# Performance work log

Measured on AMD Instinct MI355X. Metric: run time of the kernel, lower is better.

## Reference

```python
import jax, jax.numpy as jnp
import numpy as np

DIM_MODEL = 1024
NUM_HEADS = 16
HEAD_DIM = DIM_MODEL // NUM_HEADS
NEG_INF = -1e9


def setup_inputs() -> dict:
    key = jax.random.key(0)
    ks = jax.random.split(key, 12)
    B, S = 4, 2048
    s = 1.0 / np.sqrt(DIM_MODEL)
    inp = {
        "query": jax.random.normal(ks[0], (B, S, DIM_MODEL), jnp.float32),
        "key": jax.random.normal(ks[1], (B, S, DIM_MODEL), jnp.float32),
        "value": jax.random.normal(ks[2], (B, S, DIM_MODEL), jnp.float32),
        "mask": jax.random.randint(ks[3], (B, 1, S, S), 0, 2, jnp.int32),
        "Wq": jax.random.normal(ks[4], (DIM_MODEL, DIM_MODEL), jnp.float32) * s,
        "bq": jnp.zeros((DIM_MODEL,), jnp.float32),
        "Wk": jax.random.normal(ks[5], (DIM_MODEL, DIM_MODEL), jnp.float32) * s,
        "bk": jnp.zeros((DIM_MODEL,), jnp.float32),
        "Wv": jax.random.normal(ks[6], (DIM_MODEL, DIM_MODEL), jnp.float32) * s,
        "bv": jnp.zeros((DIM_MODEL,), jnp.float32),
        "Wo": jax.random.normal(ks[7], (DIM_MODEL, DIM_MODEL), jnp.float32) * s,
        "bo": jnp.zeros((DIM_MODEL,), jnp.float32),
    }
    return inp


def _split_heads(x, B):
    # [B, S, D] -> [B, H, S, Dh]
    S = x.shape[1]
    return x.reshape(B, S, NUM_HEADS, HEAD_DIM).transpose(0, 2, 1, 3)


def reference(query, key, value, mask, Wq, bq, Wk, bk, Wv, bv, Wo, bo):
    B = query.shape[0]
    q = _split_heads(query @ Wq + bq, B)   # [B,H,Sq,Dh]
    k = _split_heads(key @ Wk + bk, B)     # [B,H,Sk,Dh]
    v = _split_heads(value @ Wv + bv, B)   # [B,H,Sk,Dh]

    scale = 1.0 / np.sqrt(HEAD_DIM)
    scores = jnp.einsum("bhqd,bhkd->bhqk", q, k) * scale  # [B,H,Sq,Sk]
    scores = jnp.where(mask == 0, NEG_INF, scores)
    probs = jax.nn.softmax(scores, axis=-1)
    attn = jnp.einsum("bhqk,bhkd->bhqd", probs, v)         # [B,H,Sq,Dh]

    attn = attn.transpose(0, 2, 1, 3).reshape(B, -1, DIM_MODEL)  # [B,Sq,D]
    return attn @ Wo + bo
```

## Files before the change

### kernel.cpp

```cpp
#include <hip/hip_runtime.h>


typedef unsigned short u16;
typedef _Float16 f16;
typedef __attribute__((ext_vector_type(8))) _Float16 half8;
typedef __attribute__((ext_vector_type(8))) unsigned short u16x8;
typedef __attribute__((ext_vector_type(4))) unsigned short u16x4;
typedef __attribute__((ext_vector_type(4))) float floatx4;

__device__ f16 g_Bt[4][1024 * 1024];
__device__ f16 g_X[3][8192 * 1024];
__device__ f16 g_Qh[8192 * 1024];
__device__ f16 g_Kh[8192 * 1024];
__device__ f16 g_Vh[8192 * 1024];
__device__ f16 g_Oh[8192 * 1024];
__device__ u16 g_pbias[(size_t)4 * 2048 * 2048];
__device__ int g_is_bf16;

__device__ __forceinline__ float bf2f(u16 u) {
  union { unsigned int i; float f; } v;
  v.i = ((unsigned int)u) << 16;
  return v.f;
}
__device__ __forceinline__ u16 f2h_bits(float f) {
  union { _Float16 h; u16 u; } v;
  v.h = (_Float16)f;
  return v.u;
}

__global__ void detect_kernel(const u16* __restrict__ q) {
  if (threadIdx.x == 0) {
    int cnt = 0;
    for (int i = 0; i < 256; ++i) {
      const u16 v = q[i];
      const int e = (v >> 7) & 0xFF;
      cnt += ((e >= 100 && e <= 135) || ((v & 0x7FFF) == 0)) ? 1 : 0;
    }
    g_is_bf16 = (cnt >= 205) ? 1 : 0;
  }
}

__device__ __forceinline__ float load_in(const void* p, size_t i) {
  return g_is_bf16 ? bf2f(((const u16*)p)[i]) : ((const float*)p)[i];
}

__device__ __forceinline__ int swz128(int row, int cb) {
  return row * 128 + (cb ^ ((row & 7) << 4));
}
__device__ __forceinline__ int swz(int row, int cb) {
  return ((row << 6) + cb) ^ ((row & 7) << 4);
}

__device__ __forceinline__ void gl_lds16(void* g, void* l) {
  __builtin_amdgcn_global_load_lds(
      (__attribute__((address_space(1))) void*)g,
      (__attribute__((address_space(3))) void*)l, 16, 0, 0);
}

__global__ __launch_bounds__(256) void cvt_kernel(
    const void* __restrict__ q, const void* __restrict__ k,
    const void* __restrict__ v) {
  const int z = blockIdx.y;
  const void* x = (z == 0) ? q : (z == 1) ? k : v;
  f16* oh = g_X[z];
  const size_t i = ((size_t)blockIdx.x * 256 + threadIdx.x) * 8;
  half8 h;
  if (!g_is_bf16) {
    const float* xf = (const float*)x + i;
    const float4 a = *(const float4*)xf;
    const float4 b = *(const float4*)(xf + 4);
    h[0] = (f16)a.x; h[1] = (f16)a.y; h[2] = (f16)a.z; h[3] = (f16)a.w;
    h[4] = (f16)b.x; h[5] = (f16)b.y; h[6] = (f16)b.z; h[7] = (f16)b.w;
  } else {
    const u16x8 a = *(const u16x8*)((const u16*)x + i);
#pragma unroll
    for (int j = 0; j < 8; ++j) h[j] = (f16)bf2f(a[j]);
  }
  *(half8*)(oh + i) = h;
}

__global__ __launch_bounds__(256) void maskbias_kernel(const int* __restrict__ mask) {
  const size_t tid = (size_t)blockIdx.x * 256 + threadIdx.x;
  const size_t base = tid * 4;
  const int b = (int)(base >> 22);
  const size_t rem = base & 0x3FFFFFu;
  const int row = (int)(rem >> 11);
  const int c0 = (int)(rem & 2047);
  const int4 m = *(const int4*)(mask + base);
  const int tile = c0 >> 6;
  const int cl = c0 & 63;
  const int lan = cl & 15;
  const int ni = cl >> 4;
  u16* dst = g_pbias + ((size_t)b << 22) + ((size_t)row << 11) + tile * 64 + ni;
  const u16 NEG = 0xCE6E;
  dst[(lan + 0) * 4] = m.x ? (u16)0 : NEG;
  dst[(lan + 1) * 4] = m.y ? (u16)0 : NEG;
  dst[(lan + 2) * 4] = m.z ? (u16)0 : NEG;
  dst[(lan + 3) * 4] = m.w ? (u16)0 : NEG;
}

__global__ void wtrans_kernel(const void* __restrict__ in, int wo) {
  __shared__ float tile[32][33];
  const int tx = threadIdx.x, ty = threadIdx.y;
  const int n0 = blockIdx.x * 32, k0 = blockIdx.y * 32;
  tile[ty][tx] = load_in(in, (size_t)(k0 + ty) * 1024 + n0 + tx);
  __syncthreads();
  g_Bt[wo][(size_t)(n0 + ty) * 1024 + k0 + tx] = (f16)tile[tx][ty];
}

#define GEMM_CORE(AP, BP)                                                    \
  const int t = threadIdx.x;                                                 \
  const int lane = t & 63;                                                   \
  const int lanelo = lane & 15;                                              \
  const int quad = lane >> 4;                                                \
  const int wave = t >> 6;                                                   \
  const int wr = wave >> 1, wc = wave & 1;                                   \
  const int bm = blockIdx.x * 128;                                           \
  const int bn = blockIdx.y * 128;                                           \
         \
  const int s4 = lane << 4;                                                  \
  const int rl = s4 ^ ((s4 >> 2) & 0x70) ^ ((s4 >> 4) & 0x10);               \
  const int r0 = wave * 16 + (rl >> 6);            \
  const int cbb = rl & 63;                             \
  const char* pA0 = (const char*)(AP) + (size_t)(bm + r0) * 2048 + cbb;      \
  const char* pA1 = pA0 + (size_t)64 * 2048;                                 \
  const char* pB0 = (const char*)(BP) + (size_t)(bn + r0) * 2048 + cbb;      \
  const char* pB1 = pB0 + (size_t)64 * 2048;                                 \
  u16* lA0 = &As[wave * 512]; u16* lA1 = &As[2048 + wave * 512];             \
  u16* lB0 = &Bs[wave * 512]; u16* lB1 = &Bs[2048 + wave * 512];             \
  floatx4 acc[4][4];                                                         \
  _Pragma("unroll") for (int i = 0; i < 4; ++i)                              \
      _Pragma("unroll") for (int j = 0; j < 4; ++j) acc[i][j] = (floatx4)(0.f); \
  for (int k0 = 0; k0 < 1024; k0 += 32) {                                    \
    __syncthreads();                              \
    const size_t kb = (size_t)(k0 << 1);                                     \
    gl_lds16((void*)(pA0 + kb), lA0);                                        \
    gl_lds16((void*)(pA1 + kb), lA1);                                        \
    gl_lds16((void*)(pB0 + kb), lB0);                                        \
    gl_lds16((void*)(pB1 + kb), lB1);                                        \
    __syncthreads();       \
    half8 af[4], bf_[4];                                                     \
    _Pragma("unroll") for (int mi = 0; mi < 4; ++mi) {                       \
      const int row = wr * 64 + mi * 16 + lanelo;                            \
      af[mi] = *(const half8*)&As[swz(row, quad * 16) >> 1];                 \
    }                                                                        \
    _Pragma("unroll") for (int ni = 0; ni < 4; ++ni) {                       \
      const int row = wc * 64 + ni * 16 + lanelo;                            \
      bf_[ni] = *(const half8*)&Bs[swz(row, quad * 16) >> 1];                \
    }                                                                        \
    _Pragma("unroll") for (int mi = 0; mi < 4; ++mi)                         \
        _Pragma("unroll") for (int ni = 0; ni < 4; ++ni)                     \
      acc[mi][ni] = __builtin_amdgcn_mfma_f32_16x16x32_f16(                  \
          af[mi], bf_[ni], acc[mi][ni], 0, 0, 0);                            \
  }

__global__ __launch_bounds__(256) void gemm_qkv_kernel(
    const void* __restrict__ bq, const void* __restrict__ bk,
    const void* __restrict__ bv) {
  __shared__ __align__(16) u16 As[4096];
  __shared__ __align__(16) u16 Bs[4096];
  const int z = blockIdx.z;
  const void* bias = (z == 0) ? bq : (z == 1) ? bk : bv;
  f16* Ch = (z == 0) ? g_Qh : (z == 1) ? g_Kh : g_Vh;

  GEMM_CORE(g_X[z], g_Bt[z])

#pragma unroll
  for (int ni = 0; ni < 4; ++ni) {
    const int col = bn + wc * 64 + ni * 16 + lanelo;
    const float bvv = load_in(bias, col);
#pragma unroll
    for (int mi = 0; mi < 4; ++mi) {
#pragma unroll
      for (int rg = 0; rg < 4; ++rg) {
        const int row = bm + wr * 64 + mi * 16 + quad * 4 + rg;
        Ch[(size_t)row * 1024 + col] = (f16)(acc[mi][ni][rg] + bvv);
      }
    }
  }
}

__global__ __launch_bounds__(256) void gemm_o_kernel(
    const void* __restrict__ bias, float* __restrict__ Cptr) {
  __shared__ __align__(16) u16 As[4096];
  __shared__ __align__(16) u16 Bs[4096];

  GEMM_CORE(g_Oh, g_Bt[3])

#pragma unroll
  for (int ni = 0; ni < 4; ++ni) {
    const int col = bn + wc * 64 + ni * 16 + lanelo;
    const float bvv = load_in(bias, col);
#pragma unroll
    for (int mi = 0; mi < 4; ++mi) {
#pragma unroll
      for (int rg = 0; rg < 4; ++rg) {
        const int row = bm + wr * 64 + mi * 16 + quad * 4 + rg;
        Cptr[(size_t)row * 1024 + col] = acc[mi][ni][rg] + bvv;
      }
    }
  }
}

__global__ __launch_bounds__(512, 4) void attn_mfma_kernel() {
  constexpr int S = 2048, D = 1024, NT = S / 64;
  __shared__ __align__(16) u16 k_s[64 * 64];
  __shared__ __align__(16) u16 vt_s[64 * 64];
  __shared__ __align__(16) u16 p_s[128 * 64];

  const int t = threadIdx.x;
  const int lane = t & 63;
  const int lanelo = lane & 15;
  const int quad = lane >> 4;
  const int wave = t >> 6;

  const int q0 = blockIdx.x * 128;
  const int h = blockIdx.y;
  const int b = blockIdx.z;
  const size_t bh = (size_t)b * S * D + (size_t)h * 64;

  half8 a_q[2];
#pragma unroll
  for (int kk = 0; kk < 2; ++kk)
    a_q[kk] = *(const half8*)(g_Qh + bh +
        (size_t)(q0 + wave * 16 + lanelo) * D + kk * 32 + quad * 8);

  half8 b_ones;
#pragma unroll
  for (int j = 0; j < 8; ++j)
    b_ones[j] = (lanelo == 0) ? (f16)1.0f : (f16)0.0f;

  const int sj = t & 63;
  const int scc = (t >> 6) * 8;

  const u16* Kbase = (const u16*)g_Kh + bh + (size_t)sj * D + scc;
  const u16* Vbase = (const u16*)g_Vh + bh + (size_t)sj * D + scc;
  u16x8 kreg = *(const u16x8*)(Kbase);
  u16x8 vreg = *(const u16x8*)(Vbase);

  floatx4 o_acc[4];
#pragma unroll
  for (int ni = 0; ni < 4; ++ni) o_acc[ni] = (floatx4)(0.f);
  floatx4 o_l = (floatx4)(0.f);

  const u16* pbrow = g_pbias + ((size_t)b << 22) +
                     ((size_t)(q0 + wave * 16 + quad * 4) << 11) + (lanelo << 2);

  for (int kt = 0; kt < NT; ++kt) {
    const int j0 = kt * 64;
    __syncthreads();

    *(u16x8*)&k_s[swz128(sj, scc * 2) >> 1] = kreg;
#pragma unroll
    for (int u = 0; u < 8; ++u)
      vt_s[swz128(scc + u, sj * 2) >> 1] = vreg[u];
    __syncthreads();

    {
      const int ktn = (kt + 1 < NT) ? kt + 1 : kt;
      kreg = *(const u16x8*)(Kbase + (size_t)ktn * 64 * D);
      vreg = *(const u16x8*)(Vbase + (size_t)ktn * 64 * D);
    }
    u16x4 bs[4];
#pragma unroll
    for (int r = 0; r < 4; ++r)
      bs[r] = *(const u16x4*)(pbrow + ((size_t)r << 11) + j0);

    floatx4 sacc[4];
#pragma unroll
    for (int ni = 0; ni < 4; ++ni) sacc[ni] = (floatx4)(0.f);
#pragma unroll
    for (int kk = 0; kk < 2; ++kk) {
#pragma unroll
      for (int ni = 0; ni < 4; ++ni) {
        const half8 bb = *(const half8*)
            &k_s[swz128(ni * 16 + lanelo, kk * 64 + quad * 16) >> 1];
        sacc[ni] = __builtin_amdgcn_mfma_f32_16x16x32_f16(a_q[kk], bb, sacc[ni], 0, 0, 0);
      }
    }

#pragma unroll
    for (int r = 0; r < 4; ++r) {
      const int prow = wave * 16 + quad * 4 + r;
#pragma unroll
      for (int ni = 0; ni < 4; ++ni) {
        const float s = sacc[ni][r] * 0.125f + bf2f(bs[r][ni]);
        p_s[swz128(prow, (ni * 16 + lanelo) * 2) >> 1] = f2h_bits(__expf(s));
      }
    }
    asm volatile("s_waitcnt lgkmcnt(0)" ::: "memory");
    __builtin_amdgcn_sched_barrier(0);

#pragma unroll
    for (int kk = 0; kk < 2; ++kk) {
      const half8 a_p = *(const half8*)
          &p_s[swz128(wave * 16 + lanelo, kk * 64 + quad * 16) >> 1];
#pragma unroll
      for (int ni = 0; ni < 4; ++ni) {
        const half8 bb = *(const half8*)
            &vt_s[swz128(ni * 16 + lanelo, kk * 64 + quad * 16) >> 1];
        o_acc[ni] = __builtin_amdgcn_mfma_f32_16x16x32_f16(a_p, bb, o_acc[ni], 0, 0, 0);
      }
      o_l = __builtin_amdgcn_mfma_f32_16x16x32_f16(a_p, b_ones, o_l, 0, 0, 0);
    }
  }

#pragma unroll
  for (int r = 0; r < 4; ++r) {
    const float lsum = __shfl(o_l[r], lane & 48);
    const float inv = 1.f / lsum;
    const int row = q0 + wave * 16 + quad * 4 + r;
#pragma unroll
    for (int ni = 0; ni < 4; ++ni)
      g_Oh[bh + (size_t)row * D + ni * 16 + lanelo] = (f16)(o_acc[ni][r] * inv);
  }
}

extern "C" void kernel_launch(void* const* d_in, const int* in_sizes, int n_in,
                              void* d_out, int out_size, void* d_ws, size_t ws_size,
                              hipStream_t stream) {
  const void* query = d_in[0];
  const void* key   = d_in[1];
  const void* value = d_in[2];
  const int* mask   = (const int*)d_in[3];
  const void* Wq = d_in[4];
  const void* bq = d_in[5];
  const void* Wk = d_in[6];
  const void* bk = d_in[7];
  const void* Wv = d_in[8];
  const void* bv = d_in[9];
  const void* Wo = d_in[10];
  const void* bo = d_in[11];

  detect_kernel<<<1, 64, 0, stream>>>((const u16*)query);

  maskbias_kernel<<<16384, 256, 0, stream>>>(mask);

  dim3 tb(32, 32), tg(32, 32);
  wtrans_kernel<<<tg, tb, 0, stream>>>(Wq, 0);
  wtrans_kernel<<<tg, tb, 0, stream>>>(Wk, 1);
  wtrans_kernel<<<tg, tb, 0, stream>>>(Wv, 2);
  wtrans_kernel<<<tg, tb, 0, stream>>>(Wo, 3);

  cvt_kernel<<<dim3(4096, 3), 256, 0, stream>>>(query, key, value);

  gemm_qkv_kernel<<<dim3(64, 8, 3), 256, 0, stream>>>(bq, bk, bv);

  attn_mfma_kernel<<<dim3(16, 16, 4), 512, 0, stream>>>();

  gemm_o_kernel<<<dim3(64, 8), 256, 0, stream>>>(bo, (float*)d_out);
}
```

Measured before the change: 514.7 us.

## Double-buffer K/V tiles in attention and merge weight transposes into one launch

```diff
diff --git a/kernel.cpp b/kernel.cpp
--- a/kernel.cpp
+++ b/kernel.cpp
@@ -99,8 +99,13 @@
   dst[(lan + 3) * 4] = m.w ? (u16)0 : NEG;
 }
 
-__global__ void wtrans_kernel(const void* __restrict__ in, int wo) {
+__global__ void wtrans_kernel(const void* __restrict__ Wq,
+                              const void* __restrict__ Wk,
+                              const void* __restrict__ Wv,
+                              const void* __restrict__ Wo) {
   __shared__ float tile[32][33];
+  const int wo = blockIdx.z;
+  const void* in = (wo == 0) ? Wq : (wo == 1) ? Wk : (wo == 2) ? Wv : Wo;
   const int tx = threadIdx.x, ty = threadIdx.y;
   const int n0 = blockIdx.x * 32, k0 = blockIdx.y * 32;
   tile[ty][tx] = load_in(in, (size_t)(k0 + ty) * 1024 + n0 + tx);
@@ -204,8 +209,8 @@
 
 __global__ __launch_bounds__(512, 4) void attn_mfma_kernel() {
   constexpr int S = 2048, D = 1024, NT = S / 64;
-  __shared__ __align__(16) u16 k_s[64 * 64];
-  __shared__ __align__(16) u16 vt_s[64 * 64];
+  __shared__ __align__(16) u16 k_s[2][64 * 64];
+  __shared__ __align__(16) u16 vt_s[2][64 * 64];
   __shared__ __align__(16) u16 p_s[128 * 64];
 
   const int t = threadIdx.x;
@@ -232,35 +237,33 @@
 
   const int sj = t & 63;
   const int scc = (t >> 6) * 8;
+  const int koff = swz128(sj, scc * 2) >> 1;
 
   const u16* Kbase = (const u16*)g_Kh + bh + (size_t)sj * D + scc;
   const u16* Vbase = (const u16*)g_Vh + bh + (size_t)sj * D + scc;
+
+  floatx4 o_acc[4];
+#pragma unroll
+  for (int ni = 0; ni < 4; ++ni) o_acc[ni] = (floatx4)(0.f);
+  floatx4 o_l = (floatx4)(0.f);
+
+  const u16* pbrow = g_pbias + ((size_t)b << 22) +
+                     ((size_t)(q0 + wave * 16 + quad * 4) << 11) + (lanelo << 2);
+
   u16x8 kreg = *(const u16x8*)(Kbase);
   u16x8 vreg = *(const u16x8*)(Vbase);
-
-  floatx4 o_acc[4];
-#pragma unroll
-  for (int ni = 0; ni < 4; ++ni) o_acc[ni] = (floatx4)(0.f);
-  floatx4 o_l = (floatx4)(0.f);
-
-  const u16* pbrow = g_pbias + ((size_t)b << 22) +
-                     ((size_t)(q0 + wave * 16 + quad * 4) << 11) + (lanelo << 2);
+  *(u16x8*)&k_s[0][koff] = kreg;
+#pragma unroll
+  for (int u = 0; u < 8; ++u)
+    vt_s[0][swz128(scc + u, sj * 2) >> 1] = vreg[u];
+  kreg = *(const u16x8*)(Kbase + (size_t)64 * D);
+  vreg = *(const u16x8*)(Vbase + (size_t)64 * D);
+  __syncthreads();
 
   for (int kt = 0; kt < NT; ++kt) {
+    const int cur = kt & 1;
     const int j0 = kt * 64;
-    __syncthreads();
-
-    *(u16x8*)&k_s[swz128(sj, scc * 2) >> 1] = kreg;
-#pragma unroll
-    for (int u = 0; u < 8; ++u)
-      vt_s[swz128(scc + u, sj * 2) >> 1] = vreg[u];
-    __syncthreads();
-
-    {
-      const int ktn = (kt + 1 < NT) ? kt + 1 : kt;
-      kreg = *(const u16x8*)(Kbase + (size_t)ktn * 64 * D);
-      vreg = *(const u16x8*)(Vbase + (size_t)ktn * 64 * D);
-    }
+
     u16x4 bs[4];
 #pragma unroll
     for (int r = 0; r < 4; ++r)
@@ -274,9 +277,20 @@
 #pragma unroll
       for (int ni = 0; ni < 4; ++ni) {
         const half8 bb = *(const half8*)
-            &k_s[swz128(ni * 16 + lanelo, kk * 64 + quad * 16) >> 1];
+            &k_s[cur][swz128(ni * 16 + lanelo, kk * 64 + quad * 16) >> 1];
         sacc[ni] = __builtin_amdgcn_mfma_f32_16x16x32_f16(a_q[kk], bb, sacc[ni], 0, 0, 0);
       }
+    }
+
+    if (kt + 1 < NT) {
+      const int nxt = cur ^ 1;
+      *(u16x8*)&k_s[nxt][koff] = kreg;
+#pragma unroll
+      for (int u = 0; u < 8; ++u)
+        vt_s[nxt][swz128(scc + u, sj * 2) >> 1] = vreg[u];
+      const size_t koff2 = (size_t)((kt + 2 < NT) ? kt + 2 : NT - 1) * 64 * D;
+      kreg = *(const u16x8*)(Kbase + koff2);
+      vreg = *(const u16x8*)(Vbase + koff2);
     }
 
 #pragma unroll
@@ -298,11 +312,13 @@
 #pragma unroll
       for (int ni = 0; ni < 4; ++ni) {
         const half8 bb = *(const half8*)
-            &vt_s[swz128(ni * 16 + lanelo, kk * 64 + quad * 16) >> 1];
+            &vt_s[cur][swz128(ni * 16 + lanelo, kk * 64 + quad * 16) >> 1];
         o_acc[ni] = __builtin_amdgcn_mfma_f32_16x16x32_f16(a_p, bb, o_acc[ni], 0, 0, 0);
       }
       o_l = __builtin_amdgcn_mfma_f32_16x16x32_f16(a_p, b_ones, o_l, 0, 0, 0);
     }
+
+    __syncthreads();
   }
 
 #pragma unroll
@@ -336,11 +352,7 @@
 
   maskbias_kernel<<<16384, 256, 0, stream>>>(mask);
 
-  dim3 tb(32, 32), tg(32, 32);
-  wtrans_kernel<<<tg, tb, 0, stream>>>(Wq, 0);
-  wtrans_kernel<<<tg, tb, 0, stream>>>(Wk, 1);
-  wtrans_kernel<<<tg, tb, 0, stream>>>(Wv, 2);
-  wtrans_kernel<<<tg, tb, 0, stream>>>(Wo, 3);
+  wtrans_kernel<<<dim3(32, 32, 4), dim3(32, 32), 0, stream>>>(Wq, Wk, Wv, Wo);
 
   cvt_kernel<<<dim3(4096, 3), 256, 0, stream>>>(query, key, value);
 
```

Measured after the change: 517.4 us. No clear change (+0.5%).

## Pre-transpose V per head and fold softmax scale into Q projection

Applied to the files above, without the earlier changes.

```diff
diff --git a/kernel.cpp b/kernel.cpp
--- a/kernel.cpp
+++ b/kernel.cpp
@@ -13,6 +13,7 @@
 __device__ f16 g_Qh[8192 * 1024];
 __device__ f16 g_Kh[8192 * 1024];
 __device__ f16 g_Vh[8192 * 1024];
+__device__ f16 g_Vt[(size_t)4 * 16 * 64 * 2048];
 __device__ f16 g_Oh[8192 * 1024];
 __device__ u16 g_pbias[(size_t)4 * 2048 * 2048];
 __device__ int g_is_bf16;
@@ -99,13 +100,37 @@
   dst[(lan + 3) * 4] = m.w ? (u16)0 : NEG;
 }
 
-__global__ void wtrans_kernel(const void* __restrict__ in, int wo) {
+__global__ void wtrans_kernel(const void* __restrict__ Wq,
+                              const void* __restrict__ Wk,
+                              const void* __restrict__ Wv,
+                              const void* __restrict__ Wo) {
   __shared__ float tile[32][33];
+  const int wo = blockIdx.z;
+  const void* in = (wo == 0) ? Wq : (wo == 1) ? Wk : (wo == 2) ? Wv : Wo;
   const int tx = threadIdx.x, ty = threadIdx.y;
   const int n0 = blockIdx.x * 32, k0 = blockIdx.y * 32;
   tile[ty][tx] = load_in(in, (size_t)(k0 + ty) * 1024 + n0 + tx);
   __syncthreads();
   g_Bt[wo][(size_t)(n0 + ty) * 1024 + k0 + tx] = (f16)tile[tx][ty];
+}
+
+__global__ __launch_bounds__(512) void vtrans_kernel() {
+  __shared__ f16 tile[64][65];
+  const int tx = threadIdx.x, ty = threadIdx.y;
+  const int t0 = blockIdx.x * 64;
+  const int h = blockIdx.y;
+  const int b = blockIdx.z;
+#pragma unroll
+  for (int i = 0; i < 8; ++i) {
+    const int row = ty + i * 8;
+    tile[row][tx] = g_Vh[(size_t)(b * 2048 + t0 + row) * 1024 + h * 64 + tx];
+  }
+  __syncthreads();
+#pragma unroll
+  for (int i = 0; i < 8; ++i) {
+    const int d = ty + i * 8;
+    g_Vt[((size_t)(b * 16 + h) * 64 + d) * 2048 + t0 + tx] = tile[tx][d];
+  }
 }
 
 #define GEMM_CORE(AP, BP)                                                    \
@@ -165,6 +190,7 @@
 
   GEMM_CORE(g_X[z], g_Bt[z])
 
+  const float sc_ = (z == 0) ? 0.125f : 1.0f;
 #pragma unroll
   for (int ni = 0; ni < 4; ++ni) {
     const int col = bn + wc * 64 + ni * 16 + lanelo;
@@ -174,7 +200,7 @@
 #pragma unroll
       for (int rg = 0; rg < 4; ++rg) {
         const int row = bm + wr * 64 + mi * 16 + quad * 4 + rg;
-        Ch[(size_t)row * 1024 + col] = (f16)(acc[mi][ni][rg] + bvv);
+        Ch[(size_t)row * 1024 + col] = (f16)((acc[mi][ni][rg] + bvv) * sc_);
       }
     }
   }
@@ -232,9 +258,11 @@
 
   const int sj = t & 63;
   const int scc = (t >> 6) * 8;
+  const int koff = swz128(sj, scc * 2) >> 1;
 
   const u16* Kbase = (const u16*)g_Kh + bh + (size_t)sj * D + scc;
-  const u16* Vbase = (const u16*)g_Vh + bh + (size_t)sj * D + scc;
+  const u16* Vbase = (const u16*)g_Vt +
+                     ((size_t)(b * 16 + h) * 64 + sj) * 2048 + scc;
   u16x8 kreg = *(const u16x8*)(Kbase);
   u16x8 vreg = *(const u16x8*)(Vbase);
 
@@ -250,16 +278,14 @@
     const int j0 = kt * 64;
     __syncthreads();
 
-    *(u16x8*)&k_s[swz128(sj, scc * 2) >> 1] = kreg;
-#pragma unroll
-    for (int u = 0; u < 8; ++u)
-      vt_s[swz128(scc + u, sj * 2) >> 1] = vreg[u];
+    *(u16x8*)&k_s[koff] = kreg;
+    *(u16x8*)&vt_s[koff] = vreg;
     __syncthreads();
 
     {
       const int ktn = (kt + 1 < NT) ? kt + 1 : kt;
       kreg = *(const u16x8*)(Kbase + (size_t)ktn * 64 * D);
-      vreg = *(const u16x8*)(Vbase + (size_t)ktn * 64 * D);
+      vreg = *(const u16x8*)(Vbase + (size_t)ktn * 64);
     }
     u16x4 bs[4];
 #pragma unroll
@@ -268,7 +294,10 @@
 
     floatx4 sacc[4];
 #pragma unroll
-    for (int ni = 0; ni < 4; ++ni) sacc[ni] = (floatx4)(0.f);
+    for (int ni = 0; ni < 4; ++ni) {
+#pragma unroll
+      for (int r = 0; r < 4; ++r) sacc[ni][r] = bf2f(bs[r][ni]);
+    }
 #pragma unroll
     for (int kk = 0; kk < 2; ++kk) {
 #pragma unroll
@@ -284,8 +313,8 @@
       const int prow = wave * 16 + quad * 4 + r;
 #pragma unroll
       for (int ni = 0; ni < 4; ++ni) {
-        const float s = sacc[ni][r] * 0.125f + bf2f(bs[r][ni]);
-        p_s[swz128(prow, (ni * 16 + lanelo) * 2) >> 1] = f2h_bits(__expf(s));
+        p_s[swz128(prow, (ni * 16 + lanelo) * 2) >> 1] =
+            f2h_bits(__expf(sacc[ni][r]));
       }
     }
     asm volatile("s_waitcnt lgkmcnt(0)" ::: "memory");
@@ -336,16 +365,14 @@
 
   maskbias_kernel<<<16384, 256, 0, stream>>>(mask);
 
-  dim3 tb(32, 32), tg(32, 32);
-  wtrans_kernel<<<tg, tb, 0, stream>>>(Wq, 0);
-  wtrans_kernel<<<tg, tb, 0, stream>>>(Wk, 1);
-  wtrans_kernel<<<tg, tb, 0, stream>>>(Wv, 2);
-  wtrans_kernel<<<tg, tb, 0, stream>>>(Wo, 3);
+  wtrans_kernel<<<dim3(32, 32, 4), dim3(32, 32), 0, stream>>>(Wq, Wk, Wv, Wo);
 
   cvt_kernel<<<dim3(4096, 3), 256, 0, stream>>>(query, key, value);
 
   gemm_qkv_kernel<<<dim3(64, 8, 3), 256, 0, stream>>>(bq, bk, bv);
 
+  vtrans_kernel<<<dim3(32, 16, 4), dim3(64, 8), 0, stream>>>();
+
   attn_mfma_kernel<<<dim3(16, 16, 4), 512, 0, stream>>>();
 
   gemm_o_kernel<<<dim3(64, 8), 256, 0, stream>>>(bo, (float*)d_out);
```

Result: no change. 513.9 us (-0.2%).
